# Kernel optimization log

Measured on AMD Instinct MI355X. Metric: run time of the kernel, lower is better.

Reference implementation:

```python
import jax, jax.numpy as jnp
import numpy as np

N_EMBED = 2048
N_HEAD = 2
HEAD_SIZE = N_EMBED // N_HEAD  # 1024; mask constraint requires T <= HEAD_SIZE


def setup_inputs() -> dict:
    key = jax.random.key(0)
    ks = jax.random.split(key, 9)
    B, T, C, H, D = 32, 1024, N_EMBED, N_HEAD, HEAD_SIZE
    s = 1.0 / np.sqrt(C)
    x = jax.random.normal(ks[0], (B, T, C), dtype=jnp.float32)
    # torch Linear convention: weight (out_features, in_features), y = x @ W.T + b
    Wq = jax.random.normal(ks[1], (H, D, C), dtype=jnp.float32) * s
    Wk = jax.random.normal(ks[2], (H, D, C), dtype=jnp.float32) * s
    Wv = jax.random.normal(ks[3], (H, D, C), dtype=jnp.float32) * s
    bq = jax.random.normal(ks[4], (H, D), dtype=jnp.float32) * 0.01
    bk = jax.random.normal(ks[5], (H, D), dtype=jnp.float32) * 0.01
    bv = jax.random.normal(ks[6], (H, D), dtype=jnp.float32) * 0.01
    Wo = jax.random.normal(ks[7], (C, H * D), dtype=jnp.float32) * s  # no bias
    return {"x": x, "Wq": Wq, "bq": bq, "Wk": Wk, "bk": bk, "Wv": Wv, "bv": bv, "Wo": Wo}


def reference(x, Wq, bq, Wk, bk, Wv, bv, Wo):
    B, T, C = x.shape
    # per-head projections, batched over heads: (B,T,C) x (H,D,C) -> (B,H,T,D)
    q = jnp.einsum('btc,hdc->bhtd', x, Wq) + bq[None, :, None, :]
    k = jnp.einsum('btc,hdc->bhtd', x, Wk) + bk[None, :, None, :]
    v = jnp.einsum('btc,hdc->bhtd', x, Wv) + bv[None, :, None, :]
    # NOTE: original scales by x.shape[-1]**-0.5 == n_embed**-0.5 (not head_size)
    scale = jnp.asarray(C, x.dtype) ** -0.5
    wei = jnp.einsum('bhtd,bhsd->bhts', q, k) * scale  # (B,H,T,T)
    causal = jnp.tril(jnp.ones((T, T), dtype=bool))
    wei = jnp.where(causal[None, None], wei, -jnp.inf)
    wei = jax.nn.softmax(wei, axis=-1)
    out = jnp.einsum('bhts,bhsd->bhtd', wei, v)  # (B,H,T,D)
    # concat heads along last dim: (B,T,H*D)
    out = out.transpose(0, 2, 1, 3).reshape(B, T, -1)
    return out @ Wo.T  # (B,T,C)
```

## Files before the change

### kernel.cpp

```cpp
#include <hip/hip_runtime.h>
#include <hip/hip_bf16.h>
#include <stdint.h>

typedef __bf16 bf16_t;
typedef __bf16 bf16x8 __attribute__((ext_vector_type(8)));
typedef float f32x4 __attribute__((ext_vector_type(4)));

#define AS1(p) ((const __attribute__((address_space(1))) void*)(uintptr_t)(p))
#define AS3(p) ((__attribute__((address_space(3))) void*)(uintptr_t)(p))

__device__ __forceinline__ void gload16(const bf16_t* g, bf16_t* l) {
  __builtin_amdgcn_global_load_lds(AS1(g), AS3(l), 16, 0, 0);
}

#define SB()      __builtin_amdgcn_sched_barrier(0);
#define BAR()     { __builtin_amdgcn_sched_barrier(0); __builtin_amdgcn_s_barrier(); __builtin_amdgcn_sched_barrier(0); }
#define VMCNT(n)  { asm volatile("s_waitcnt vmcnt(" #n ")" ::: "memory"); __builtin_amdgcn_sched_barrier(0); }
#define LGKM(n)   { asm volatile("s_waitcnt lgkmcnt(" #n ")" ::: "memory"); __builtin_amdgcn_sched_barrier(0); }

__device__ __forceinline__ void gemm256(const bf16_t* __restrict__ A, int lda,
                                        const bf16_t* __restrict__ B, int ldb,
                                        int nt, f32x4 acc[8][4], bf16_t* lds) {
  const int t = (int)threadIdx.x;
  const int lane = t & 63, w = t >> 6;
  const int wr = w >> 2, wc = w & 3;
  const int fr = lane & 15, fq = lane >> 4;
  char* ldsb = (char*)lds;

  const int s0 = (t * 16) ^ (((t >> 3) & 7) << 4);
  const int r0 = s0 >> 6, q0 = (s0 >> 4) & 3;
  const bf16_t* gA0 = A + (size_t)r0 * lda + q0 * 8;
  const bf16_t* gA1 = gA0 + (size_t)128 * lda;
  const bf16_t* gB0 = B + (size_t)r0 * ldb + q0 * 8;
  const bf16_t* gB1 = gB0 + (size_t)128 * ldb;

  const int swz = (fr * 64 + fq * 16) ^ (((fr >> 1) & 7) << 4);
  const int abase = wr * 8192 + swz;
  const int bbase = 32768 + wc * 4096 + swz;

  bf16x8 bb[4], aa0[4], aa1[4];

#define STAGE_A(cb, kh, kof) { \
    bf16_t* _d = lds + (cb) * 32768 + (kh) * 8192; \
    gload16(gA0 + (kof) + (kh) * 32, _d + t * 8); \
    gload16(gA1 + (kof) + (kh) * 32, _d + 4096 + t * 8); \
  } SB()
#define STAGE_B(cb, kh, kof) { \
    bf16_t* _d = lds + (cb) * 32768 + 16384 + (kh) * 8192; \
    gload16(gB0 + (kof) + (kh) * 32, _d + t * 8); \
    gload16(gB1 + (kof) + (kh) * 32, _d + 4096 + t * 8); \
  } SB()
#define READ_B(cb, kh) { \
    const char* _b = ldsb + (cb) * 65536 + (kh) * 16384 + bbase; \
    _Pragma("unroll") for (int n = 0; n < 4; ++n) bb[n] = *(const bf16x8*)(_b + n * 1024); }
#define READ_A(cb, kh, qm, dst) { \
    const char* _a = ldsb + (cb) * 65536 + (kh) * 16384 + abase + (qm) * 4096; \
    _Pragma("unroll") for (int i = 0; i < 4; ++i) dst[i] = *(const bf16x8*)(_a + i * 1024); }
#define MFMA16(dst, qm) { \
    __builtin_amdgcn_s_setprio(1); \
    _Pragma("unroll") for (int i = 0; i < 4; ++i) \
      _Pragma("unroll") for (int n = 0; n < 4; ++n) \
        acc[(qm) * 4 + i][n] = __builtin_amdgcn_mfma_f32_16x16x32_bf16(dst[i], bb[n], acc[(qm) * 4 + i][n], 0, 0, 0); \
    __builtin_amdgcn_s_setprio(0); }

  STAGE_A(0, 0, 0) STAGE_B(0, 0, 0) STAGE_A(0, 1, 0) STAGE_B(0, 1, 0)

  int kof = 64;
  for (int tt = 0; tt < nt - 1; ++tt, kof += 64) {
    const int cb = tt & 1;
    VMCNT(4) BAR()
    READ_B(cb, 0) READ_A(cb, 0, 0, aa0)
    STAGE_A(cb ^ 1, 0, kof)
    READ_A(cb, 0, 1, aa1)
    STAGE_B(cb ^ 1, 0, kof)
    LGKM(4) MFMA16(aa0, 0)
    LGKM(0) MFMA16(aa1, 1)
    VMCNT(4) BAR()
    READ_B(cb, 1) READ_A(cb, 1, 0, aa0)
    STAGE_A(cb ^ 1, 1, kof)
    READ_A(cb, 1, 1, aa1)
    STAGE_B(cb ^ 1, 1, kof)
    LGKM(4) MFMA16(aa0, 0)
    LGKM(0) MFMA16(aa1, 1)
  }
  {
    const int cb = (nt - 1) & 1;
    VMCNT(4) BAR()
    READ_B(cb, 0) READ_A(cb, 0, 0, aa0) READ_A(cb, 0, 1, aa1)
    LGKM(4) MFMA16(aa0, 0)
    LGKM(0) MFMA16(aa1, 1)
    VMCNT(0) BAR()
    READ_B(cb, 1) READ_A(cb, 1, 0, aa0) READ_A(cb, 1, 1, aa1)
    LGKM(4) MFMA16(aa0, 0)
    LGKM(0) MFMA16(aa1, 1)
  }
#undef STAGE_A
#undef STAGE_B
#undef READ_B
#undef READ_A
#undef MFMA16
}

#define EPI_VARS \
  const int t = (int)threadIdx.x; \
  const int lane = t & 63, w = t >> 6; \
  const int wr = w >> 2, wc = w & 3; \
  const int fr = lane & 15, fq = lane >> 4;

#define ZERO8x4(acc) \
  _Pragma("unroll") for (int _i = 0; _i < 8; ++_i) \
  _Pragma("unroll") for (int _j = 0; _j < 4; ++_j) { f32x4 _z = {0.f,0.f,0.f,0.f}; acc[_i][_j] = _z; }

__global__ void k_cvt(const float* __restrict__ s, bf16_t* __restrict__ d, long n8) {
  long i = (long)blockIdx.x * blockDim.x + threadIdx.x;
  long st = (long)gridDim.x * blockDim.x;
  for (; i < n8; i += st) {
    const float4* sp = (const float4*)(s + i * 8);
    float4 a = sp[0], b = sp[1];
    bf16x8 v;
    v[0] = (__bf16)a.x; v[1] = (__bf16)a.y; v[2] = (__bf16)a.z; v[3] = (__bf16)a.w;
    v[4] = (__bf16)b.x; v[5] = (__bf16)b.y; v[6] = (__bf16)b.z; v[7] = (__bf16)b.w;
    *(bf16x8*)(d + i * 8) = v;
  }
}

__global__ void k_fill(float* o, float v, long n) {
  long i = (long)blockIdx.x * blockDim.x + threadIdx.x;
  long st = (long)gridDim.x * blockDim.x;
  for (; i < n; i += st) o[i] = v;
}

__global__ __launch_bounds__(512, 2) void k_qkv256(
    const bf16_t* __restrict__ xb, const bf16_t* __restrict__ Wb,
    const float* __restrict__ bq, const float* __restrict__ bk, const float* __restrict__ bv,
    bf16_t* __restrict__ Q, bf16_t* __restrict__ K, bf16_t* __restrict__ Vt) {
  __shared__ __align__(16) bf16_t lds[65536];
  int bid = (int)blockIdx.x;
  int id = (bid & 7) * 384 + (bid >> 3);
  EPI_VARS
  f32x4 acc[8][4];
  ZERO8x4(acc)

  bool vmode = id >= 2048;
  int mt = 0, ntile = 0, tok = 0, wm = 0;
  const bf16_t *Ap, *Bp;
  if (!vmode) {
    mt = id & 127; ntile = id >> 7;
    Ap = xb + (size_t)mt * 256 * 2048;
    Bp = Wb + (size_t)ntile * 256 * 2048;
  } else {
    int vb = id - 2048;
    tok = vb & 127; wm = vb >> 7;
    Ap = Wb + (size_t)(16 + wm) * 256 * 2048;
    Bp = xb + (size_t)tok * 256 * 2048;
  }
  gemm256(Ap, 2048, Bp, 2048, 32, acc, lds);

  if (!vmode) {
    int sel = ntile >> 3;
    const float* bias = sel ? bk : bq;
    bf16_t* dst = sel ? K : Q;
    int cbase = (ntile & 7) * 256 + wc * 64;
#pragma unroll
    for (int ni = 0; ni < 4; ++ni) {
      int c2 = cbase + ni * 16 + fr;
      int h = c2 >> 10, d = c2 & 1023;
      float bb = bias[c2];
#pragma unroll
      for (int mi = 0; mi < 8; ++mi) {
        f32x4 a = acc[mi][ni];
#pragma unroll
        for (int r = 0; r < 4; ++r) {
          int m = mt * 256 + wr * 128 + mi * 16 + fq * 4 + r;
          int b = m >> 10, tk = m & 1023;
          dst[(((size_t)(b * 2 + h) << 10) + tk) * 1024 + d] = (bf16_t)(a[r] + bb);
        }
      }
    }
  } else {
#pragma unroll
    for (int mi = 0; mi < 8; ++mi) {
#pragma unroll
      for (int r = 0; r < 4; ++r) {
        int gd = wm * 256 + wr * 128 + mi * 16 + fq * 4 + r;
        int h = gd >> 10, dd = gd & 1023;
        float bb = bv[gd];
#pragma unroll
        for (int ni = 0; ni < 4; ++ni) {
          int m = tok * 256 + wc * 64 + ni * 16 + fr;
          int b = m >> 10, tk = m & 1023;
          Vt[(((size_t)(b * 2 + h) << 10) + dd) * 1024 + tk] = (bf16_t)(acc[mi][ni][r] + bb);
        }
      }
    }
  }
}

__global__ __launch_bounds__(512, 2) void k_s256(const bf16_t* __restrict__ Q,
                                                 const bf16_t* __restrict__ K,
                                                 bf16_t* __restrict__ S, int pbase) {
  __shared__ __align__(16) bf16_t lds[65536];
  int id = (int)blockIdx.x;
  int pc = id / 10, rem = id % 10;
  int ti = 0;
  while (rem > ti) { rem -= ti + 1; ++ti; }
  int tj = rem;
  size_t p = (size_t)(pbase + pc);
  EPI_VARS
  f32x4 acc[8][4];
  ZERO8x4(acc)
  gemm256(Q + (p << 20) + (size_t)ti * 256 * 1024, 1024,
          K + (p << 20) + (size_t)tj * 256 * 1024, 1024, 16, acc, lds);
  bf16_t* Sp = S + ((size_t)pc << 20);
  const float scale = 0.022097086912079608f;
#pragma unroll
  for (int mi = 0; mi < 8; ++mi)
#pragma unroll
    for (int ni = 0; ni < 4; ++ni) {
      int col = tj * 256 + wc * 64 + ni * 16 + fr;
      f32x4 a = acc[mi][ni];
#pragma unroll
      for (int r = 0; r < 4; ++r) {
        int row = ti * 256 + wr * 128 + mi * 16 + fq * 4 + r;
        Sp[((size_t)row << 10) + col] = (bf16_t)(a[r] * scale);
      }
    }
}

__global__ __launch_bounds__(256) void k_softmax(const bf16_t* __restrict__ S,
                                                 bf16_t* __restrict__ P) {
  int gw = (int)blockIdx.x * 4 + ((int)threadIdx.x >> 6);
  int pc = gw >> 10, row = gw & 1023;
  int lane = (int)threadIdx.x & 63;
  const bf16_t* s = S + ((size_t)pc << 20) + ((size_t)row << 10);
  bf16_t* p = P + ((size_t)pc << 20) + ((size_t)row << 10);
  int cend = ((row >> 8) + 1) << 8;
  bf16x8 v0 = *(const bf16x8*)(s + lane * 8);
  bf16x8 v1 = *(const bf16x8*)(s + 512 + lane * 8);
  float x[16];
  float mx = -1e30f;
#pragma unroll
  for (int j = 0; j < 8; ++j) {
    int c0 = lane * 8 + j, c1 = 512 + lane * 8 + j;
    x[j]     = (c0 <= row) ? (float)v0[j] : -1e30f;
    x[8 + j] = (c1 <= row) ? (float)v1[j] : -1e30f;
    mx = fmaxf(mx, fmaxf(x[j], x[8 + j]));
  }
  for (int o = 32; o > 0; o >>= 1) mx = fmaxf(mx, __shfl_xor(mx, o));
  float sum = 0.f;
#pragma unroll
  for (int j = 0; j < 16; ++j) {
    x[j] = (x[j] > -1e29f) ? __expf(x[j] - mx) : 0.f;
    sum += x[j];
  }
  for (int o = 32; o > 0; o >>= 1) sum += __shfl_xor(sum, o);
  float inv = 1.f / sum;
  bf16x8 o0, o1;
#pragma unroll
  for (int j = 0; j < 8; ++j) {
    o0[j] = (bf16_t)(x[j] * inv);
    o1[j] = (bf16_t)(x[8 + j] * inv);
  }
  if (lane * 8 < cend)       *(bf16x8*)(p + lane * 8) = o0;
  if (512 + lane * 8 < cend) *(bf16x8*)(p + 512 + lane * 8) = o1;
}

__global__ __launch_bounds__(512, 2) void k_pv256(const bf16_t* __restrict__ P,
                                                  const bf16_t* __restrict__ Vt,
                                                  bf16_t* __restrict__ O, int pbase) {
  __shared__ __align__(16) bf16_t lds[65536];
  int id = (int)blockIdx.x;
  int pc = id >> 4, rem = id & 15;
  int ti = rem >> 2, dj = rem & 3;
  size_t p = (size_t)(pbase + pc);
  EPI_VARS
  f32x4 acc[8][4];
  ZERO8x4(acc)
  gemm256(P + ((size_t)pc << 20) + (size_t)ti * 256 * 1024, 1024,
          Vt + (p << 20) + (size_t)dj * 256 * 1024, 1024, (ti + 1) * 4, acc, lds);
  int b = (int)(p >> 1), h = (int)(p & 1);
#pragma unroll
  for (int mi = 0; mi < 8; ++mi)
#pragma unroll
    for (int ni = 0; ni < 4; ++ni) {
      int dcol = dj * 256 + wc * 64 + ni * 16 + fr;
      f32x4 a = acc[mi][ni];
#pragma unroll
      for (int r = 0; r < 4; ++r) {
        int tk = ti * 256 + wr * 128 + mi * 16 + fq * 4 + r;
        O[(((size_t)b << 10) + tk) * 2048 + (h << 10) + dcol] = (bf16_t)a[r];
      }
    }
}

__global__ __launch_bounds__(512, 2) void k_out256(const bf16_t* __restrict__ O,
                                                   const bf16_t* __restrict__ W,
                                                   float* __restrict__ out) {
  __shared__ __align__(16) bf16_t lds[65536];
  int bid = (int)blockIdx.x;
  int id = (bid & 7) * 128 + (bid >> 3);
  int mt = id & 127, ntile = id >> 7;
  EPI_VARS
  f32x4 acc[8][4];
  ZERO8x4(acc)
  gemm256(O + (size_t)mt * 256 * 2048, 2048, W + (size_t)ntile * 256 * 2048, 2048, 32, acc, lds);
#pragma unroll
  for (int mi = 0; mi < 8; ++mi)
#pragma unroll
    for (int ni = 0; ni < 4; ++ni) {
      int col = ntile * 256 + wc * 64 + ni * 16 + fr;
      f32x4 a = acc[mi][ni];
#pragma unroll
      for (int r = 0; r < 4; ++r) {
        int row = mt * 256 + wr * 128 + mi * 16 + fq * 4 + r;
        out[(size_t)row * 2048 + col] = a[r];
      }
    }
}

extern "C" void kernel_launch(void* const* d_in, const int* in_sizes, int n_in,
                              void* d_out, int out_size, void* d_ws, size_t ws_size,
                              hipStream_t stream) {
  const float* x  = (const float*)d_in[0];
  const float* Wq = (const float*)d_in[1];
  const float* bq = (const float*)d_in[2];
  const float* Wk = (const float*)d_in[3];
  const float* bk = (const float*)d_in[4];
  const float* Wv = (const float*)d_in[5];
  const float* bv = (const float*)d_in[6];
  const float* Wo = (const float*)d_in[7];
  float* out = (float*)d_out;

  const size_t MiB = 1ull << 20;
  char* w = (char*)d_ws;
  bf16_t* xb    = (bf16_t*)w;
  bf16_t* Ob    = xb;
  bf16_t* Qb    = (bf16_t*)(w + 128 * MiB);
  bf16_t* Kb    = (bf16_t*)(w + 256 * MiB);
  bf16_t* Vt    = (bf16_t*)(w + 384 * MiB);
  bf16_t* Wqkvb = (bf16_t*)(w + 512 * MiB);
  bf16_t* Wob   = (bf16_t*)(w + 536 * MiB);
  bf16_t* Sc    = (bf16_t*)(w + 544 * MiB);

  size_t rem = ws_size > 544 * MiB ? ws_size - 544 * MiB : 0;
  int NP = (int)(rem / (4 * MiB));
  if (NP > 64) NP = 64;
  if (NP < 1) {
    k_fill<<<2048, 256, 0, stream>>>(out, (float)(ws_size >> 20), (long)out_size);
    return;
  }
  bf16_t* Pc = (bf16_t*)(w + 544 * MiB + (size_t)NP * 2 * MiB);

  k_cvt<<<2048, 256, 0, stream>>>(x, xb, 8388608L);
  k_cvt<<<1024, 256, 0, stream>>>(Wq, Wqkvb, 524288L);
  k_cvt<<<1024, 256, 0, stream>>>(Wk, Wqkvb + 4194304, 524288L);
  k_cvt<<<1024, 256, 0, stream>>>(Wv, Wqkvb + 8388608, 524288L);
  k_cvt<<<1024, 256, 0, stream>>>(Wo, Wob, 524288L);

  k_qkv256<<<3072, 512, 0, stream>>>(xb, Wqkvb, bq, bk, bv, Qb, Kb, Vt);

  for (int base = 0; base < 64; base += NP) {
    int np = (64 - base) < NP ? (64 - base) : NP;
    k_s256<<<np * 10, 512, 0, stream>>>(Qb, Kb, Sc, base);
    k_softmax<<<np * 256, 256, 0, stream>>>(Sc, Pc);
    k_pv256<<<np * 16, 512, 0, stream>>>(Pc, Vt, Ob, base);
  }

  k_out256<<<1024, 512, 0, stream>>>(Ob, Wob, out);
}
```

Before: 1.475 ms.

## Pre-pack weights into MFMA fragment order and load them directly to registers

Adds a packing kernel that converts Wq, Wk and Wo to bf16 in an MFMA-fragment-ordered layout. A new GEMM variant loads the B (weight) operand straight from global memory into registers and stages only A through LDS, for the Q/K projections and the output projection. This removes LDS traffic and staging for the weight operand and shrinks LDS use in k_out256. In exchange, each wave issues global loads for B with fewer bytes in flight per barrier, and reuse of B across the workgroup now relies on cache. The sched_barrier before each s_barrier is also removed.

```diff
diff --git a/kernel.cpp b/kernel.cpp
--- a/kernel.cpp
+++ b/kernel.cpp
@@ -14,7 +14,7 @@
 }
 
 #define SB()      __builtin_amdgcn_sched_barrier(0);
-#define BAR()     { __builtin_amdgcn_sched_barrier(0); __builtin_amdgcn_s_barrier(); __builtin_amdgcn_sched_barrier(0); }
+#define BARR()    { __builtin_amdgcn_s_barrier(); __builtin_amdgcn_sched_barrier(0); }
 #define VMCNT(n)  { asm volatile("s_waitcnt vmcnt(" #n ")" ::: "memory"); __builtin_amdgcn_sched_barrier(0); }
 #define LGKM(n)   { asm volatile("s_waitcnt lgkmcnt(" #n ")" ::: "memory"); __builtin_amdgcn_sched_barrier(0); }
 
@@ -22,8 +22,8 @@
                                         const bf16_t* __restrict__ B, int ldb,
                                         int nt, f32x4 acc[8][4], bf16_t* lds) {
   const int t = (int)threadIdx.x;
-  const int lane = t & 63, w = t >> 6;
-  const int wr = w >> 2, wc = w & 3;
+  const int lane = t & 63, wv = t >> 6;
+  const int wr = wv >> 2, wc = wv & 3;
   const int fr = lane & 15, fq = lane >> 4;
   char* ldsb = (char*)lds;
 
@@ -68,14 +68,14 @@
   int kof = 64;
   for (int tt = 0; tt < nt - 1; ++tt, kof += 64) {
     const int cb = tt & 1;
-    VMCNT(4) BAR()
+    VMCNT(4) BARR()
     READ_B(cb, 0) READ_A(cb, 0, 0, aa0)
     STAGE_A(cb ^ 1, 0, kof)
     READ_A(cb, 0, 1, aa1)
     STAGE_B(cb ^ 1, 0, kof)
     LGKM(4) MFMA16(aa0, 0)
     LGKM(0) MFMA16(aa1, 1)
-    VMCNT(4) BAR()
+    VMCNT(4) BARR()
     READ_B(cb, 1) READ_A(cb, 1, 0, aa0)
     STAGE_A(cb ^ 1, 1, kof)
     READ_A(cb, 1, 1, aa1)
@@ -85,11 +85,11 @@
   }
   {
     const int cb = (nt - 1) & 1;
-    VMCNT(4) BAR()
+    VMCNT(4) BARR()
     READ_B(cb, 0) READ_A(cb, 0, 0, aa0) READ_A(cb, 0, 1, aa1)
     LGKM(4) MFMA16(aa0, 0)
     LGKM(0) MFMA16(aa1, 1)
-    VMCNT(0) BAR()
+    VMCNT(0) BARR()
     READ_B(cb, 1) READ_A(cb, 1, 0, aa0) READ_A(cb, 1, 1, aa1)
     LGKM(4) MFMA16(aa0, 0)
     LGKM(0) MFMA16(aa1, 1)
@@ -99,6 +99,78 @@
 #undef READ_B
 #undef READ_A
 #undef MFMA16
+}
+
+__device__ __forceinline__ void gemm256w(const bf16_t* __restrict__ A, int lda,
+                                         const bf16_t* __restrict__ Bp,
+                                         int H, f32x4 acc[8][4], bf16_t* lds) {
+  const int t = (int)threadIdx.x;
+  const int lane = t & 63, wv = t >> 6;
+  const int wr = wv >> 2, wc = wv & 3;
+  const int fr = lane & 15, fq = lane >> 4;
+  char* ldsb = (char*)lds;
+
+  const int s0 = (t * 16) ^ (((t >> 3) & 7) << 4);
+  const int r0 = s0 >> 6, q0 = (s0 >> 4) & 3;
+  const bf16_t* gA0 = A + (size_t)r0 * lda + q0 * 8;
+  const bf16_t* gA1 = gA0 + (size_t)128 * lda;
+
+  const int swz = (fr * 64 + fq * 16) ^ (((fr >> 1) & 7) << 4);
+  const int abase = wr * 8192 + swz;
+  const bf16_t* gBp = Bp + wc * 2048 + lane * 8;
+
+  bf16x8 aa0[4], aa1[4], bbA[4], bbB[4];
+
+#define WSTAGE_A(buf, kof) { \
+    bf16_t* _d = lds + (buf) * 8192; \
+    gload16(gA0 + (kof), _d + t * 8); \
+    gload16(gA1 + (kof), _d + 4096 + t * 8); \
+  } SB()
+#define WLOADB(set, w) { \
+    const bf16_t* _b = gBp + (size_t)(w) * 8192; \
+    _Pragma("unroll") for (int n = 0; n < 4; ++n) set[n] = *(const bf16x8*)(_b + n * 512); }
+#define WREAD_A(buf, qm, dst) { \
+    const char* _a = ldsb + (buf) * 16384 + abase + (qm) * 4096; \
+    _Pragma("unroll") for (int i = 0; i < 4; ++i) dst[i] = *(const bf16x8*)(_a + i * 1024); }
+#define WMFMA(dst, qm, bset) { \
+    _Pragma("unroll") for (int i = 0; i < 4; ++i) \
+      _Pragma("unroll") for (int n = 0; n < 4; ++n) \
+        acc[(qm) * 4 + i][n] = __builtin_amdgcn_mfma_f32_16x16x32_bf16(dst[i], bset[n], acc[(qm) * 4 + i][n], 0, 0, 0); }
+
+  WSTAGE_A(0, 0) WLOADB(bbA, 0)
+  int w = 0;
+  for (; w + 2 < H; w += 2) {
+    VMCNT(0) BARR()
+    WREAD_A(0, 0, aa0)
+    WSTAGE_A(1, (w + 1) * 32) WLOADB(bbB, w + 1)
+    WREAD_A(0, 1, aa1)
+    LGKM(4)
+    __builtin_amdgcn_s_setprio(1); WMFMA(aa0, 0, bbA)
+    LGKM(0) WMFMA(aa1, 1, bbA) __builtin_amdgcn_s_setprio(0);
+    VMCNT(0) BARR()
+    WREAD_A(1, 0, aa0)
+    WSTAGE_A(0, (w + 2) * 32) WLOADB(bbA, w + 2)
+    WREAD_A(1, 1, aa1)
+    LGKM(4)
+    __builtin_amdgcn_s_setprio(1); WMFMA(aa0, 0, bbB)
+    LGKM(0) WMFMA(aa1, 1, bbB) __builtin_amdgcn_s_setprio(0);
+  }
+  VMCNT(0) BARR()
+  WREAD_A(0, 0, aa0)
+  WSTAGE_A(1, (H - 1) * 32) WLOADB(bbB, H - 1)
+  WREAD_A(0, 1, aa1)
+  LGKM(4)
+  __builtin_amdgcn_s_setprio(1); WMFMA(aa0, 0, bbA)
+  LGKM(0) WMFMA(aa1, 1, bbA) __builtin_amdgcn_s_setprio(0);
+  VMCNT(0) BARR()
+  WREAD_A(1, 0, aa0) WREAD_A(1, 1, aa1)
+  LGKM(4)
+  __builtin_amdgcn_s_setprio(1); WMFMA(aa0, 0, bbB)
+  LGKM(0) WMFMA(aa1, 1, bbB) __builtin_amdgcn_s_setprio(0);
+#undef WSTAGE_A
+#undef WLOADB
+#undef WREAD_A
+#undef WMFMA
 }
 
 #define EPI_VARS \
@@ -124,6 +196,26 @@
   }
 }
 
+__global__ void k_packw(const float* __restrict__ Wsrc, bf16_t* __restrict__ dst, long nunits) {
+  long o = (long)blockIdx.x * blockDim.x + threadIdx.x;
+  long st = (long)gridDim.x * blockDim.x;
+  for (; o < nunits; o += st) {
+    int lane = (int)(o & 63);
+    long r = o >> 6;
+    int cgrp = (int)(r & 15); r >>= 4;
+    int kh = (int)(r & 63);
+    long nt = r >> 6;
+    int col = (int)nt * 256 + cgrp * 16 + (lane & 15);
+    int k = kh * 32 + (lane >> 4) * 8;
+    const float* s = Wsrc + (size_t)col * 2048 + k;
+    float4 a = ((const float4*)s)[0], b = ((const float4*)s)[1];
+    bf16x8 v;
+    v[0] = (__bf16)a.x; v[1] = (__bf16)a.y; v[2] = (__bf16)a.z; v[3] = (__bf16)a.w;
+    v[4] = (__bf16)b.x; v[5] = (__bf16)b.y; v[6] = (__bf16)b.z; v[7] = (__bf16)b.w;
+    *(bf16x8*)(dst + o * 8) = v;
+  }
+}
+
 __global__ void k_fill(float* o, float v, long n) {
   long i = (long)blockIdx.x * blockDim.x + threadIdx.x;
   long st = (long)gridDim.x * blockDim.x;
@@ -131,7 +223,8 @@
 }
 
 __global__ __launch_bounds__(512, 2) void k_qkv256(
-    const bf16_t* __restrict__ xb, const bf16_t* __restrict__ Wb,
+    const bf16_t* __restrict__ xb, const bf16_t* __restrict__ Wvb,
+    const bf16_t* __restrict__ Wpqk,
     const float* __restrict__ bq, const float* __restrict__ bk, const float* __restrict__ bv,
     bf16_t* __restrict__ Q, bf16_t* __restrict__ K, bf16_t* __restrict__ Vt) {
   __shared__ __align__(16) bf16_t lds[65536];
@@ -142,21 +235,10 @@
   ZERO8x4(acc)
 
   bool vmode = id >= 2048;
-  int mt = 0, ntile = 0, tok = 0, wm = 0;
-  const bf16_t *Ap, *Bp;
   if (!vmode) {
-    mt = id & 127; ntile = id >> 7;
-    Ap = xb + (size_t)mt * 256 * 2048;
-    Bp = Wb + (size_t)ntile * 256 * 2048;
-  } else {
-    int vb = id - 2048;
-    tok = vb & 127; wm = vb >> 7;
-    Ap = Wb + (size_t)(16 + wm) * 256 * 2048;
-    Bp = xb + (size_t)tok * 256 * 2048;
-  }
-  gemm256(Ap, 2048, Bp, 2048, 32, acc, lds);
-
-  if (!vmode) {
+    int mt = id & 127, ntile = id >> 7;
+    gemm256w(xb + (size_t)mt * 256 * 2048, 2048,
+             Wpqk + (size_t)ntile * 524288, 64, acc, lds);
     int sel = ntile >> 3;
     const float* bias = sel ? bk : bq;
     bf16_t* dst = sel ? K : Q;
@@ -178,6 +260,10 @@
       }
     }
   } else {
+    int vb = id - 2048;
+    int tok = vb & 127, wm = vb >> 7;
+    gemm256(Wvb + (size_t)wm * 256 * 2048, 2048,
+            xb + (size_t)tok * 256 * 2048, 2048, 32, acc, lds);
 #pragma unroll
     for (int mi = 0; mi < 8; ++mi) {
 #pragma unroll
@@ -294,16 +380,17 @@
 }
 
 __global__ __launch_bounds__(512, 2) void k_out256(const bf16_t* __restrict__ O,
-                                                   const bf16_t* __restrict__ W,
+                                                   const bf16_t* __restrict__ Wpo,
                                                    float* __restrict__ out) {
-  __shared__ __align__(16) bf16_t lds[65536];
+  __shared__ __align__(16) bf16_t lds[16384];
   int bid = (int)blockIdx.x;
   int id = (bid & 7) * 128 + (bid >> 3);
   int mt = id & 127, ntile = id >> 7;
   EPI_VARS
   f32x4 acc[8][4];
   ZERO8x4(acc)
-  gemm256(O + (size_t)mt * 256 * 2048, 2048, W + (size_t)ntile * 256 * 2048, 2048, 32, acc, lds);
+  gemm256w(O + (size_t)mt * 256 * 2048, 2048,
+           Wpo + (size_t)ntile * 524288, 64, acc, lds);
 #pragma unroll
   for (int mi = 0; mi < 8; ++mi)
 #pragma unroll
@@ -338,8 +425,9 @@
   bf16_t* Qb    = (bf16_t*)(w + 128 * MiB);
   bf16_t* Kb    = (bf16_t*)(w + 256 * MiB);
   bf16_t* Vt    = (bf16_t*)(w + 384 * MiB);
-  bf16_t* Wqkvb = (bf16_t*)(w + 512 * MiB);
-  bf16_t* Wob   = (bf16_t*)(w + 536 * MiB);
+  bf16_t* Wvb   = (bf16_t*)(w + 512 * MiB);
+  bf16_t* Wpqk  = (bf16_t*)(w + 520 * MiB);
+  bf16_t* Wpo   = (bf16_t*)(w + 536 * MiB);
   bf16_t* Sc    = (bf16_t*)(w + 544 * MiB);
 
   size_t rem = ws_size > 544 * MiB ? ws_size - 544 * MiB : 0;
@@ -352,12 +440,12 @@
   bf16_t* Pc = (bf16_t*)(w + 544 * MiB + (size_t)NP * 2 * MiB);
 
   k_cvt<<<2048, 256, 0, stream>>>(x, xb, 8388608L);
-  k_cvt<<<1024, 256, 0, stream>>>(Wq, Wqkvb, 524288L);
-  k_cvt<<<1024, 256, 0, stream>>>(Wk, Wqkvb + 4194304, 524288L);
-  k_cvt<<<1024, 256, 0, stream>>>(Wv, Wqkvb + 8388608, 524288L);
-  k_cvt<<<1024, 256, 0, stream>>>(Wo, Wob, 524288L);
-
-  k_qkv256<<<3072, 512, 0, stream>>>(xb, Wqkvb, bq, bk, bv, Qb, Kb, Vt);
+  k_cvt<<<1024, 256, 0, stream>>>(Wv, Wvb, 524288L);
+  k_packw<<<1024, 256, 0, stream>>>(Wq, Wpqk, 524288L);
+  k_packw<<<1024, 256, 0, stream>>>(Wk, Wpqk + 4194304, 524288L);
+  k_packw<<<1024, 256, 0, stream>>>(Wo, Wpo, 524288L);
+
+  k_qkv256<<<3072, 512, 0, stream>>>(xb, Wvb, Wpqk, bq, bk, bv, Qb, Kb, Vt);
 
   for (int base = 0; base < 64; base += NP) {
     int np = (64 - base) < NP ? (64 - base) : NP;
@@ -366,5 +454,5 @@
     k_pv256<<<np * 16, 512, 0, stream>>>(Pc, Vt, Ob, base);
   }
 
-  k_out256<<<1024, 512, 0, stream>>>(Ob, Wob, out);
-}
+  k_out256<<<1024, 512, 0, stream>>>(Ob, Wpo, out);
+}
```

New measurement: 1.723 ms. 1.17x slower.
